# Kernel tuning notes

Hardware: AMD Instinct MI355X
Metric: run time of the kernel (lower is better)

Reference implementation:

```python
import jax, jax.numpy as jnp
import numpy as np

B, N, E = 16, 8192, 131072
CIN, H, HL, C = 128, 128, 128, 10
K1 = -(-N // 2)    # ceil(0.5 * 8192) = 4096 nodes kept after pool1
K2 = -(-K1 // 2)   # ceil(0.5 * 4096) = 2048 nodes kept after pool2


def setup_inputs() -> dict:
    key = jax.random.key(0)
    ks = jax.random.split(key, 12)

    def w(k, shape, fan):
        return (jax.random.normal(k, shape, jnp.float32) / np.sqrt(fan)).astype(jnp.float32)

    return {
        "x": jax.random.normal(ks[0], (B, N, CIN), jnp.float32),
        "edge_index": jax.random.randint(ks[1], (B, 2, E), 0, N),
        "W1": w(ks[2], (CIN, H), CIN), "b1": jnp.zeros((H,), jnp.float32),
        "p1_wrel": w(ks[3], (H, 1), H), "p1_wroot": w(ks[4], (H, 1), H), "p1_b": jnp.zeros((1,), jnp.float32),
        "W2": w(ks[5], (H, H), H), "b2": jnp.zeros((H,), jnp.float32),
        "p2_wrel": w(ks[6], (H, 1), H), "p2_wroot": w(ks[7], (H, 1), H), "p2_b": jnp.zeros((1,), jnp.float32),
        "W3": w(ks[8], (H, H), H), "b3": jnp.zeros((H,), jnp.float32),
        "lin1_w": w(ks[9], (H, HL), H), "lin1_b": jnp.zeros((HL,), jnp.float32),
        "lin2_w": w(ks[10], (HL, C), HL), "lin2_b": jnp.zeros((C,), jnp.float32),
    }


def _gcn(x, src, dst, mask, W, b):
    # GCNConv with self-loops + symmetric deg^-1/2 normalization on the
    # mask-induced subgraph (removed nodes contribute zero edge weight).
    ew = mask[src] * mask[dst]                                    # [E]
    deg = jax.ops.segment_sum(ew, dst, num_segments=N) + mask     # self-loop weight = mask
    deg_safe = jnp.where(deg > 0, deg, 1.0)
    dinv = jnp.where(deg > 0, jax.lax.rsqrt(deg_safe), 0.0)
    xw = x @ W                                                    # [N,H]
    norm = dinv[src] * ew * dinv[dst]                             # [E]
    agg = jax.ops.segment_sum(xw[src] * norm[:, None], dst, num_segments=N)
    out = agg + xw * (dinv * dinv * mask)[:, None] + b
    return out * mask[:, None]


def _sag_pool(x, src, dst, mask, wrel, wroot, bb, k):
    # SAGPooling: GraphConv(H,1) score (sum aggregation), top-k over live
    # nodes, tanh-gated features. Node filtering == updating the mask.
    ew = mask[src] * mask[dst]
    agg = jax.ops.segment_sum(x[src] * ew[:, None], dst, num_segments=N)
    score = (agg @ wrel + x @ wroot + bb)[:, 0] * mask            # [N]
    _, idx = jax.lax.top_k(jnp.where(mask > 0, score, -jnp.inf), k)
    new_mask = jnp.zeros((N,), x.dtype).at[idx].set(1.0)
    return x * jnp.tanh(score)[:, None] * new_mask[:, None], new_mask


def reference(x, edge_index, W1, b1, p1_wrel, p1_wroot, p1_b,
              W2, b2, p2_wrel, p2_wroot, p2_b, W3, b3,
              lin1_w, lin1_b, lin2_w, lin2_b):
    def per_graph(xg, ei):
        src, dst = ei[0], ei[1]
        mask = jnp.ones((N,), xg.dtype)
        h = jax.nn.relu(_gcn(xg, src, dst, mask, W1, b1))
        h, mask = _sag_pool(h, src, dst, mask, p1_wrel, p1_wroot, p1_b, K1)
        h = jax.nn.relu(_gcn(h, src, dst, mask, W2, b2))
        h, mask = _sag_pool(h, src, dst, mask, p2_wrel, p2_wroot, p2_b, K2)
        h = jax.nn.relu(_gcn(h, src, dst, mask, W3, b3))
        return h.sum(0) / K2  # global mean pool over the K2 surviving nodes

    g = jax.vmap(per_graph)(x, edge_index)                        # [B,H]
    hh = jax.nn.relu(g @ lin1_w + lin1_b)
    logits = hh @ lin2_w + lin2_b
    return jax.nn.log_softmax(logits, axis=-1)
```

## Files before the change

kernel.cpp:

```cpp
#include <hip/hip_runtime.h>
#include <hip/hip_bf16.h>
#include <math.h>

constexpr int B  = 16;
constexpr int N  = 8192;
constexpr int E  = 131072;
constexpr int H  = 128;
constexpr int K1 = 4096;
constexpr int K2 = 2048;

constexpr int CHUNKS = 16;
constexpr int NBK    = 16;
constexpr int FCAP   = 12288;

typedef __attribute__((ext_vector_type(8))) short short8;
typedef __attribute__((ext_vector_type(4))) float floatx4;

__device__ __forceinline__ unsigned short f2bf(float f) {
  unsigned u = __float_as_uint(f);
  return (unsigned short)((u + 0x7FFFu + ((u >> 16) & 1u)) >> 16);
}
__device__ __forceinline__ float bf2f(unsigned short s) {
  return __uint_as_float(((unsigned)s) << 16);
}
__device__ __forceinline__ int rdlane_i(int v, int l) {
  return __builtin_amdgcn_readlane(v, l);
}
__device__ __forceinline__ float rdlane_f(float v, int l) {
  return __uint_as_float((unsigned)__builtin_amdgcn_readlane((int)__float_as_uint(v), l));
}
__device__ __forceinline__ unsigned cvt_pk_bf16(float a, float b) {
  unsigned r;
  asm("v_cvt_pk_bf16_f32 %0, %1, %2" : "=v"(r) : "v"(a), "v"(b));
  return r;
}

__global__ __launch_bounds__(256) void hist_pass(const int* __restrict__ ei,
                                                 int* __restrict__ bchist) {
  int blk = blockIdx.x;
  int b = blk >> 4, c = blk & 15;
  __shared__ int h16[NBK];
  if (threadIdx.x < NBK) h16[threadIdx.x] = 0;
  __syncthreads();
  const int* dstp = ei + (size_t)b * 2 * E + E + c * 8192;
  for (int i = 0; i < 32; ++i) {
    int dst = dstp[i * 256 + threadIdx.x];
    atomicAdd(&h16[dst >> 9], 1);
  }
  __syncthreads();
  if (threadIdx.x < NBK) bchist[(blk << 4) + threadIdx.x] = h16[threadIdx.x];
}

__global__ __launch_bounds__(256) void bucket_scan(const int* __restrict__ bchist,
                                                   int* __restrict__ cursor,
                                                   int* __restrict__ bbase,
                                                   const float* __restrict__ W1,
                                                   const float* __restrict__ W2,
                                                   const float* __restrict__ W3,
                                                   unsigned short* __restrict__ Wt) {
  if (blockIdx.x >= 16) {
    int w = blockIdx.x - 16;
    const float* W = (w == 0) ? W1 : (w == 1) ? W2 : W3;
    unsigned short* o = Wt + w * 128 * 128;
    for (int i = threadIdx.x; i < 128 * 128; i += 256) {
      int k = i >> 7, n = i & 127;
      o[n * 128 + k] = f2bf(W[i]);
    }
    return;
  }
  int b = blockIdx.x;
  int tid = threadIdx.x;
  int c = tid >> 4, k = tid & 15;
  __shared__ int arr[CHUNKS][NBK];
  __shared__ int base[NBK + 1];
  arr[c][k] = bchist[((b * CHUNKS + c) << 4) + k];
  __syncthreads();
  if (tid == 0) {
    int run = 0;
    for (int kk = 0; kk < NBK; ++kk) {
      base[kk] = run;
      int t = 0;
      for (int cc = 0; cc < CHUNKS; ++cc) t += arr[cc][kk];
      run += t;
    }
    base[NBK] = run;
  }
  __syncthreads();
  int pre = 0;
  for (int cc = 0; cc < c; ++cc) pre += arr[cc][k];
  cursor[((b * CHUNKS + c) << 4) + k] = base[k] + pre;
  if (tid < NBK + 1) bbase[b * (NBK + 1) + tid] = base[tid];
}

__global__ __launch_bounds__(256) void bin_scatter(const int* __restrict__ ei,
                                                   const int* __restrict__ cursor,
                                                   unsigned* __restrict__ pbuf) {
  int blk = blockIdx.x;
  int b = blk >> 4, c = blk & 15;
  __shared__ int gcur[NBK], lcnt[NBK], lfill[NBK];
  __shared__ int lbase[NBK + 1];
  __shared__ unsigned sbuf[2048];
  int tid = threadIdx.x;
  if (tid < NBK) gcur[tid] = cursor[(blk << 4) + tid];
  const int* srcp = ei + (size_t)b * 2 * E + c * 8192;
  const int* dstp = srcp + E;
  unsigned* pb = pbuf + (size_t)b * E;

  for (int sc = 0; sc < 4; ++sc) {
    if (tid < NBK) { lcnt[tid] = 0; lfill[tid] = 0; }
    __syncthreads();
    int s8[8], d8[8];
#pragma unroll
    for (int q = 0; q < 8; ++q) {
      int i = sc * 2048 + q * 256 + tid;
      s8[q] = srcp[i]; d8[q] = dstp[i];
      atomicAdd(&lcnt[d8[q] >> 9], 1);
    }
    __syncthreads();
    if (tid == 0) {
      int run = 0;
      for (int k = 0; k < NBK; ++k) { lbase[k] = run; run += lcnt[k]; }
      lbase[NBK] = run;
    }
    __syncthreads();
#pragma unroll
    for (int q = 0; q < 8; ++q) {
      int k = d8[q] >> 9;
      int idx = atomicAdd(&lfill[k], 1);
      sbuf[lbase[k] + idx] = ((unsigned)k << 22) |
                             ((unsigned)(d8[q] & 511) << 13) | (unsigned)s8[q];
    }
    __syncthreads();
    for (int i = tid; i < 2048; i += 256) {
      unsigned pk = sbuf[i];
      int k = (int)(pk >> 22);
      pb[gcur[k] + (i - lbase[k])] = pk;
    }
    __syncthreads();
    if (tid < NBK) gcur[tid] += lcnt[tid];
    __syncthreads();
  }
}

__global__ __launch_bounds__(256) void final_scatter(const unsigned* __restrict__ pbuf,
                                                     const int* __restrict__ bbase,
                                                     int* __restrict__ csr,
                                                     int* __restrict__ offs,
                                                     float* __restrict__ dinv1) {
  int blk = blockIdx.x;
  int b = blk >> 4, k = blk & 15;
  __shared__ int ncnt[512], nbase[512], nfill[512];
  __shared__ int sred[256];
  __shared__ unsigned sbuf[FCAP];
  int tid = threadIdx.x;
  int gbase = bbase[b * (NBK + 1) + k];
  int gend  = bbase[b * (NBK + 1) + k + 1];
  int cnt = gend - gbase;
  const unsigned* pb = pbuf + (size_t)b * E + gbase;

  for (int i = tid; i < 512; i += 256) { ncnt[i] = 0; nfill[i] = 0; }
  __syncthreads();
  for (int i = tid; i < cnt; i += 256) atomicAdd(&ncnt[(pb[i] >> 13) & 511], 1);
  __syncthreads();
  int v0 = ncnt[2 * tid], v1 = ncnt[2 * tid + 1];
  int s = v0 + v1;
  sred[tid] = s;
  __syncthreads();
  for (int off = 1; off < 256; off <<= 1) {
    int x = (tid >= off) ? sred[tid - off] : 0;
    __syncthreads();
    sred[tid] += x;
    __syncthreads();
  }
  int ex = sred[tid] - s;
  nbase[2 * tid] = ex;
  nbase[2 * tid + 1] = ex + v0;
  __syncthreads();
  for (int i = tid; i < 512; i += 256) {
    int node = k * 512 + i;
    offs[b * (N + 1) + node] = gbase + nbase[i];
    dinv1[b * N + node] = rsqrtf((float)ncnt[i] + 1.0f);
  }
  if (k == 15 && tid == 0) offs[b * (N + 1) + N] = E;
  __syncthreads();
  for (int i = tid; i < cnt; i += 256) {
    unsigned pk = pb[i];
    int node = (pk >> 13) & 511;
    int idx = atomicAdd(&nfill[node], 1);
    sbuf[nbase[node] + idx] = pk & 8191u;
  }
  __syncthreads();
  int* co = csr + (size_t)b * E + gbase;
  for (int i = tid; i < cnt; i += 256) co[i] = (int)sbuf[i];
}

template <bool ABF16>
__global__ __launch_bounds__(256) void gemm_mfma(const void* __restrict__ Ap,
                                                 const unsigned short* __restrict__ Wt,
                                                 unsigned short* __restrict__ Cb,
                                                 const float* __restrict__ fscale,
                                                 const float* __restrict__ dscale) {
  __shared__ unsigned short Wsh[128 * 128];
  int tid  = threadIdx.x;
  int lane = tid & 63;
  int l15  = lane & 15, lg = lane >> 4;
  size_t rowbase = (size_t)blockIdx.x * 128 + (tid >> 6) * 32;

#pragma unroll
  for (int i = 0; i < 8; ++i) {
    int idx = tid + i * 256;
    int row = idx >> 4, s = idx & 15;
    short8 v = *(const short8*)(Wt + idx * 8);
    *(short8*)(Wsh + row * 128 + (s ^ (row & 15)) * 8) = v;
  }

  short8 afrag[2][4];
#pragma unroll
  for (int rg = 0; rg < 2; ++rg) {
    size_t row = rowbase + rg * 16 + l15;
#pragma unroll
    for (int c = 0; c < 4; ++c) {
      int k0 = c * 32 + lg * 8;
      if (ABF16) {
        afrag[rg][c] = *(const short8*)((const unsigned short*)Ap + row * 128 + k0);
      } else {
        const float* p = (const float*)Ap + row * 128 + k0;
        float4 v0 = *(const float4*)p;
        float4 v1 = *(const float4*)(p + 4);
        short8 a;
        a[0] = (short)f2bf(v0.x); a[1] = (short)f2bf(v0.y);
        a[2] = (short)f2bf(v0.z); a[3] = (short)f2bf(v0.w);
        a[4] = (short)f2bf(v1.x); a[5] = (short)f2bf(v1.y);
        a[6] = (short)f2bf(v1.z); a[7] = (short)f2bf(v1.w);
        afrag[rg][c] = a;
      }
    }
  }

  float fsr0[4] = {1.f, 1.f, 1.f, 1.f}, fsr1[4] = {1.f, 1.f, 1.f, 1.f};
  if (fscale != nullptr) {
    float4 t0 = *(const float4*)(fscale + rowbase + lg * 4);
    float4 t1 = *(const float4*)(fscale + rowbase + 16 + lg * 4);
    fsr0[0] = t0.x; fsr0[1] = t0.y; fsr0[2] = t0.z; fsr0[3] = t0.w;
    fsr1[0] = t1.x; fsr1[1] = t1.y; fsr1[2] = t1.z; fsr1[3] = t1.w;
  }
  if (dscale != nullptr) {
    float4 t0 = *(const float4*)(dscale + rowbase + lg * 4);
    float4 t1 = *(const float4*)(dscale + rowbase + 16 + lg * 4);
    fsr0[0] *= t0.x; fsr0[1] *= t0.y; fsr0[2] *= t0.z; fsr0[3] *= t0.w;
    fsr1[0] *= t1.x; fsr1[1] *= t1.y; fsr1[2] *= t1.z; fsr1[3] *= t1.w;
  }

  __syncthreads();

#pragma unroll
  for (int t = 0; t < 8; ++t) {
    int col = t * 16 + l15;
    short8 bfrag[4];
#pragma unroll
    for (int c = 0; c < 4; ++c)
      bfrag[c] = *(const short8*)(Wsh + col * 128 + ((c * 4 + lg) ^ (col & 15)) * 8);

    floatx4 acc0 = {0.f, 0.f, 0.f, 0.f};
    floatx4 acc1 = {0.f, 0.f, 0.f, 0.f};
#pragma unroll
    for (int c = 0; c < 4; ++c) {
      acc0 = __builtin_amdgcn_mfma_f32_16x16x32_bf16(afrag[0][c], bfrag[c], acc0, 0, 0, 0);
      acc1 = __builtin_amdgcn_mfma_f32_16x16x32_bf16(afrag[1][c], bfrag[c], acc1, 0, 0, 0);
    }
#pragma unroll
    for (int r = 0; r < 4; ++r) {
      size_t row0 = rowbase + lg * 4 + r;
      size_t row1 = rowbase + 16 + lg * 4 + r;
      Cb[row0 * 128 + col] = f2bf(acc0[r] * fsr0[r]);
      Cb[row1 * 128 + col] = f2bf(acc1[r] * fsr1[r]);
    }
  }
}

template <bool ALL_LIVE>
__global__ __launch_bounds__(256) void gcn_agg8(
    const unsigned* __restrict__ tmp, const float* __restrict__ dinv,
    const int* __restrict__ offs, const int* __restrict__ ecnt,
    const int* __restrict__ csr, const float* __restrict__ bias,
    unsigned* __restrict__ hout,
    const float* __restrict__ wrel, const float* __restrict__ wroot,
    float* __restrict__ rr, float* __restrict__ tt) {
  int blk = blockIdx.x;
  int xcd = blk & 7;
  int j   = blk >> 3;
  int b   = xcd * 2 + (j >> 11);
  int n   = (j & 2047) * 4 + (threadIdx.x >> 6);
  int wid = b * N + n;
  int lane = threadIdx.x & 63;

  float dv = rdlane_f(dinv[wid], 0);
  unsigned* hrow = hout + (size_t)wid * 64;

  if (!ALL_LIVE && dv <= 0.0f) {
    hrow[lane] = 0u;
    if (rr != nullptr && lane == 0) { rr[wid] = 0.0f; tt[wid] = 0.0f; }
    return;
  }

  const unsigned* tmpb = tmp + (((size_t)b << 13) << 6);
  const int* cs = csr + (size_t)b * E;

  float2 accA, accB;
  {
    unsigned u = tmpb[((unsigned)n << 6) + lane];
    accA.x = __uint_as_float(u << 16);
    accA.y = __uint_as_float(u & 0xFFFF0000u);
    accB.x = 0.0f; accB.y = 0.0f;
  }

  int nbase = b * (N + 1) + n;
  int o0 = __builtin_amdgcn_readfirstlane(offs[nbase]);
  int d;
  if (ALL_LIVE) d = __builtin_amdgcn_readfirstlane(offs[nbase + 1]) - o0;
  else          d = __builtin_amdgcn_readfirstlane(ecnt[wid]);

  for (int base = 0; base < d; base += 64) {
    int nv = d - base; if (nv > 64) nv = 64;
    int sl = (lane < nv) ? cs[o0 + base + lane] : 0;

    int nfull = nv >> 4;
    for (int t = 0; t < nfull; ++t) {
      int i0 = t << 4;
      unsigned uu[16];
#pragma unroll
      for (int q = 0; q < 16; ++q) {
        int sq = rdlane_i(sl, i0 + q);
        uu[q] = tmpb[((unsigned)sq << 6) + lane];
      }
#pragma unroll
      for (int q = 0; q < 16; ++q) {
        float lo = __uint_as_float(uu[q] << 16);
        float hi = __uint_as_float(uu[q] & 0xFFFF0000u);
        if (q & 1) { accB.x += lo; accB.y += hi; }
        else       { accA.x += lo; accA.y += hi; }
      }
    }
    int rem = nv & 15;
    if (rem) {
      int i0 = nfull << 4;
      unsigned uu[16];
#pragma unroll
      for (int q = 0; q < 16; ++q) {
        int idx = i0 + q;
        int sq = rdlane_i(sl, idx < nv ? idx : 0);
        unsigned v = tmpb[((unsigned)sq << 6) + lane];
        uu[q] = (idx < nv) ? v : 0u;
      }
#pragma unroll
      for (int q = 0; q < 16; ++q) {
        float lo = __uint_as_float(uu[q] << 16);
        float hi = __uint_as_float(uu[q] & 0xFFFF0000u);
        if (q & 1) { accB.x += lo; accB.y += hi; }
        else       { accA.x += lo; accA.y += hi; }
      }
    }
  }

  float2 acc = {accA.x + accB.x, accA.y + accB.y};
  const float2 bb = *(const float2*)(bias + lane * 2);
  float2 outv;
  outv.x = fmaxf(dv * acc.x + bb.x, 0.0f);
  outv.y = fmaxf(dv * acc.y + bb.y, 0.0f);
  hrow[lane] = cvt_pk_bf16(outv.x, outv.y);

  if (rr != nullptr) {
    const float2 wr = *(const float2*)(wrel + lane * 2);
    const float2 wo = *(const float2*)(wroot + lane * 2);
    float pr = outv.x * wr.x + outv.y * wr.y;
    float pt = outv.x * wo.x + outv.y * wo.y;
#pragma unroll
    for (int dd = 32; dd > 0; dd >>= 1) {
      pr += __shfl_down(pr, dd);
      pt += __shfl_down(pt, dd);
    }
    if (lane == 0) { rr[wid] = pr; tt[wid] = pt; }
  }
}

__global__ __launch_bounds__(256) void compact_pool(
    const float* __restrict__ mask, const int* __restrict__ offs,
    const int* __restrict__ ecnt_in, int* __restrict__ csr,
    int* __restrict__ ecnt_out, float* __restrict__ dinv_out) {
  int wid = blockIdx.x * 4 + (threadIdx.x >> 6);
  int lane = threadIdx.x & 63;
  int b = wid >> 13, n = wid & (N - 1);
  float m = rdlane_f(mask[wid], 0);
  if (m <= 0.0f) {
    if (lane == 0) { ecnt_out[wid] = 0; dinv_out[wid] = 0.0f; }
    return;
  }
  int nb = b * (N + 1) + n;
  int o0 = __builtin_amdgcn_readfirstlane(offs[nb]);
  int din = (ecnt_in != nullptr)
                ? __builtin_amdgcn_readfirstlane(ecnt_in[wid])
                : __builtin_amdgcn_readfirstlane(offs[nb + 1]) - o0;
  int* cs = csr + (size_t)b * E;
  const float* mb = mask + b * N;
  int wpos = o0;
  for (int base = 0; base < din; base += 64) {
    int nv = din - base; if (nv > 64) nv = 64;
    int s = (lane < nv) ? cs[o0 + base + lane] : 0;
    bool alive = (lane < nv) && (mb[s] > 0.0f);
    unsigned long long bal = __ballot(alive);
    int idx = __popcll(bal & ((1ull << lane) - 1ull));
    if (alive) cs[wpos + idx] = s;
    wpos += __popcll(bal);
  }
  if (lane == 0) {
    int total = wpos - o0;
    ecnt_out[wid] = total;
    dinv_out[wid] = rsqrtf((float)total + 1.0f);
  }
}

__global__ __launch_bounds__(256) void score_agg(const float* __restrict__ r,
                                                 const float* __restrict__ t,
                                                 const float* __restrict__ pb,
                                                 const float* __restrict__ livep,
                                                 const int* __restrict__ offs,
                                                 const int* __restrict__ ecnt,
                                                 const int* __restrict__ csr,
                                                 float* __restrict__ score) {
  int grp = threadIdx.x >> 4;
  int gl  = threadIdx.x & 15;
  int nid = blockIdx.x * 16 + grp;
  int b = nid >> 13, n = nid & (N - 1);
  bool live = (livep == nullptr) || (livep[nid] > 0.0f);
  float s = 0.0f;
  if (live) {
    int o0 = offs[b * (N + 1) + n];
    int d = (ecnt != nullptr) ? ecnt[nid] : offs[b * (N + 1) + n + 1] - o0;
    const int* cs = csr + (size_t)b * E;
    const float* rb = r + b * N;
    for (int base = 0; base < d; base += 16)
      if (base + gl < d) s += rb[cs[o0 + base + gl]];
  }
#pragma unroll
  for (int dd = 8; dd > 0; dd >>= 1) s += __shfl_xor(s, dd, 16);
  if (gl == 0) score[nid] = live ? (s + t[nid] + pb[0]) : 0.0f;
}

__device__ __forceinline__ unsigned fkey(float s, float m) {
  if (m <= 0.0f) return 0u;
  unsigned u = __float_as_uint(s);
  return (u & 0x80000000u) ? ~u : (u | 0x80000000u);
}

__global__ __launch_bounds__(1024) void topk_kernel(const float* __restrict__ score,
                                                    const float* __restrict__ mkin,
                                                    float* __restrict__ mkout,
                                                    float* __restrict__ fscale,
                                                    int k) {
  int b = blockIdx.x, tid = threadIdx.x;
  const float* sc = score + b * N;
  float* mk = mkout + b * N;
  float* fs = fscale + b * N;
  __shared__ unsigned keyb[N];
  __shared__ int hist[256];
  __shared__ unsigned sh_prefix;
  __shared__ int sh_kneed;
  __shared__ int wsum[16], wexc[16];

  for (int i = tid; i < N; i += 1024) {
    float m = (mkin == nullptr) ? 1.0f : mkin[b * N + i];
    keyb[i] = fkey(sc[i], m);
  }
  __syncthreads();

  unsigned prefix = 0, hm = 0;
  int kneed = k;
  for (int shift = 24; shift >= 0; shift -= 8) {
    if (tid < 256) hist[tid] = 0;
    __syncthreads();
    for (int i = tid; i < N; i += 1024) {
      unsigned key = keyb[i];
      if ((key & hm) == prefix) atomicAdd(&hist[(key >> shift) & 255], 1);
    }
    __syncthreads();
    if (tid < 64) {
      int b4[4]; int s = 0;
#pragma unroll
      for (int j = 0; j < 4; ++j) { b4[j] = hist[tid * 4 + j]; s += b4[j]; }
      int suf = s;
#pragma unroll
      for (int o = 1; o < 64; o <<= 1) {
        int v = __shfl_down(suf, o);
        if (tid + o < 64) suf += v;
      }
      int run = suf - s;
      for (int j = 3; j >= 0; --j) {
        if (run < kneed && run + b4[j] >= kneed) {
          sh_prefix = prefix | ((unsigned)(tid * 4 + j) << shift);
          sh_kneed = kneed - run;
        }
        run += b4[j];
      }
    }
    __syncthreads();
    prefix = sh_prefix;
    kneed = sh_kneed;
    hm |= (0xFFu << shift);
  }

  unsigned T = prefix;
  int base = tid * 8;
  unsigned keys[8];
  int eqf[8];
  int cnt = 0;
#pragma unroll
  for (int q = 0; q < 8; ++q) {
    keys[q] = keyb[base + q];
    eqf[q] = (keys[q] == T) ? 1 : 0;
    cnt += eqf[q];
  }
  int inc = cnt;
  int wl = tid & 63;
#pragma unroll
  for (int o = 1; o < 64; o <<= 1) {
    int v = __shfl_up(inc, o);
    if (wl >= o) inc += v;
  }
  if (wl == 63) wsum[tid >> 6] = inc;
  __syncthreads();
  if (tid < 16) {
    int v = wsum[tid];
    int in = v;
#pragma unroll
    for (int o = 1; o < 16; o <<= 1) {
      int u = __shfl_up(in, o);
      if (tid >= o) in += u;
    }
    wexc[tid] = in - v;
  }
  __syncthreads();
  int ex = wexc[tid >> 6] + (inc - cnt);
#pragma unroll
  for (int q = 0; q < 8; ++q) {
    bool sel = (keys[q] > T) || (eqf[q] && (ex < kneed));
    ex += eqf[q];
    mk[base + q] = sel ? 1.0f : 0.0f;
    fs[base + q] = sel ? tanhf(sc[base + q]) : 0.0f;
  }
}

__global__ __launch_bounds__(256) void readout(const unsigned short* __restrict__ h,
                                               float* __restrict__ part) {
  int b = blockIdx.x, c = blockIdx.y;
  int tid = threadIdx.x;
  int f = tid & 127, half = tid >> 7;
  float acc = 0.0f;
  for (int n = c * 256 + half; n < (c + 1) * 256; n += 2)
    acc += bf2f(h[((size_t)b * N + n) * 128 + f]);
  __shared__ float red[256];
  red[tid] = acc; __syncthreads();
  if (half == 0) part[((size_t)b * 32 + c) * 128 + f] = red[f] + red[f + 128];
}

__global__ __launch_bounds__(128) void head(const float* __restrict__ part,
                                            const float* __restrict__ l1w,
                                            const float* __restrict__ l1b,
                                            const float* __restrict__ l2w,
                                            const float* __restrict__ l2b,
                                            float* __restrict__ out) {
  int b = blockIdx.x, f = threadIdx.x;
  float g = 0.0f;
  for (int c = 0; c < 32; ++c) g += part[((size_t)b * 32 + c) * 128 + f];
  g *= (1.0f / (float)K2);
  __shared__ float gs[128], hh[128], lg[10];
  gs[f] = g; __syncthreads();
  float a = l1b[f];
  for (int kk = 0; kk < 128; ++kk) a += gs[kk] * l1w[kk * 128 + f];
  hh[f] = fmaxf(a, 0.0f); __syncthreads();
  if (f < 10) {
    float l = l2b[f];
    for (int j = 0; j < 128; ++j) l += hh[j] * l2w[j * 10 + f];
    lg[f] = l;
  }
  __syncthreads();
  if (f == 0) {
    float m = lg[0];
    for (int c = 1; c < 10; ++c) m = fmaxf(m, lg[c]);
    float s = 0.0f;
    for (int c = 0; c < 10; ++c) s += expf(lg[c] - m);
    float lse = m + logf(s);
    for (int c = 0; c < 10; ++c) out[b * 10 + c] = lg[c] - lse;
  }
}

extern "C" void kernel_launch(void* const* d_in, const int* in_sizes, int n_in,
                              void* d_out, int out_size, void* d_ws, size_t ws_size,
                              hipStream_t stream) {
  (void)in_sizes; (void)n_in; (void)out_size; (void)ws_size;
  const float* x       = (const float*)d_in[0];
  const int*   ei      = (const int*)d_in[1];
  const float* W1      = (const float*)d_in[2];
  const float* b1      = (const float*)d_in[3];
  const float* p1_wrel = (const float*)d_in[4];
  const float* p1_wroot= (const float*)d_in[5];
  const float* p1_b    = (const float*)d_in[6];
  const float* W2      = (const float*)d_in[7];
  const float* b2      = (const float*)d_in[8];
  const float* p2_wrel = (const float*)d_in[9];
  const float* p2_wroot= (const float*)d_in[10];
  const float* p2_b    = (const float*)d_in[11];
  const float* W3      = (const float*)d_in[12];
  const float* b3      = (const float*)d_in[13];
  const float* l1w     = (const float*)d_in[14];
  const float* l1b     = (const float*)d_in[15];
  const float* l2w     = (const float*)d_in[16];
  const float* l2b     = (const float*)d_in[17];
  float* out = (float*)d_out;

  char* p = (char*)d_ws;
  auto alloc = [&](size_t bytes) {
    char* r = p;
    p += ((bytes + 255) & ~(size_t)255);
    return r;
  };
  unsigned short* h   = (unsigned short*)alloc((size_t)B * N * H * 2);
  unsigned short* tmp = (unsigned short*)alloc((size_t)B * N * H * 2);
  int*      offs   = (int*)alloc((size_t)B * (N + 1) * 4);
  int*      csr    = (int*)alloc((size_t)B * E * 4);
  unsigned* pbuf   = (unsigned*)alloc((size_t)B * E * 4);
  int*      bchist = (int*)alloc((size_t)B * CHUNKS * NBK * 4);
  int*      cursor = (int*)alloc((size_t)B * CHUNKS * NBK * 4);
  int*      bbase  = (int*)alloc((size_t)B * (NBK + 1) * 4);
  int*      ecnt   = (int*)alloc((size_t)B * N * 4);
  float* dinv   = (float*)alloc((size_t)B * N * 4);
  float* mask   = (float*)alloc((size_t)B * N * 4);
  float* rr     = (float*)alloc((size_t)B * N * 4);
  float* tt     = (float*)alloc((size_t)B * N * 4);
  float* score  = (float*)alloc((size_t)B * N * 4);
  float* fscale = (float*)alloc((size_t)B * N * 4);
  float* part   = (float*)alloc((size_t)B * 32 * H * 4);
  unsigned short* Wts = (unsigned short*)alloc(3 * 128 * 128 * 2);

  hist_pass<<<B * CHUNKS, 256, 0, stream>>>(ei, bchist);
  bucket_scan<<<19, 256, 0, stream>>>(bchist, cursor, bbase, W1, W2, W3, Wts);
  bin_scatter<<<B * CHUNKS, 256, 0, stream>>>(ei, cursor, pbuf);
  final_scatter<<<B * NBK, 256, 0, stream>>>(pbuf, bbase, csr, offs, dinv);

  gemm_mfma<false><<<(B * N) / 128, 256, 0, stream>>>(x, Wts, tmp, nullptr, dinv);
  gcn_agg8<true><<<B * N / 4, 256, 0, stream>>>((const unsigned*)tmp, dinv, offs,
                                                nullptr, csr, b1, (unsigned*)h,
                                                p1_wrel, p1_wroot, rr, tt);
  score_agg<<<B * N / 16, 256, 0, stream>>>(rr, tt, p1_b, nullptr, offs, nullptr,
                                            csr, score);
  topk_kernel<<<B, 1024, 0, stream>>>(score, nullptr, mask, fscale, K1);
  compact_pool<<<B * N / 4, 256, 0, stream>>>(mask, offs, nullptr, csr, ecnt, dinv);

  gemm_mfma<true><<<(B * N) / 128, 256, 0, stream>>>(h, Wts + 128 * 128, tmp,
                                                     fscale, dinv);
  gcn_agg8<false><<<B * N / 4, 256, 0, stream>>>((const unsigned*)tmp, dinv, offs,
                                                 ecnt, csr, b2, (unsigned*)h,
                                                 p2_wrel, p2_wroot, rr, tt);
  score_agg<<<B * N / 16, 256, 0, stream>>>(rr, tt, p2_b, dinv, offs, ecnt, csr, score);
  topk_kernel<<<B, 1024, 0, stream>>>(score, mask, mask, fscale, K2);
  compact_pool<<<B * N / 4, 256, 0, stream>>>(mask, offs, ecnt, csr, ecnt, dinv);

  gemm_mfma<true><<<(B * N) / 128, 256, 0, stream>>>(h, Wts + 2 * 128 * 128, tmp,
                                                     fscale, dinv);
  gcn_agg8<false><<<B * N / 4, 256, 0, stream>>>((const unsigned*)tmp, dinv, offs,
                                                 ecnt, csr, b3, (unsigned*)h,
                                                 nullptr, nullptr, nullptr, nullptr);

  readout<<<dim3(B, 32), 256, 0, stream>>>(h, part);
  head<<<B, 128, 0, stream>>>(part, l1w, l1b, l2w, l2b, out);
}
```

Measured before the change: 392.4 us.

## Launch pooled stages only over surviving nodes via top-k index lists

```diff
diff --git a/kernel.cpp b/kernel.cpp
--- a/kernel.cpp
+++ b/kernel.cpp
@@ -194,12 +194,10 @@
   for (int i = tid; i < cnt; i += 256) co[i] = (int)sbuf[i];
 }
 
-template <bool ABF16>
-__global__ __launch_bounds__(256) void gemm_mfma(const void* __restrict__ Ap,
-                                                 const unsigned short* __restrict__ Wt,
-                                                 unsigned short* __restrict__ Cb,
-                                                 const float* __restrict__ fscale,
-                                                 const float* __restrict__ dscale) {
+__global__ __launch_bounds__(256) void gemm_l1(const float* __restrict__ Ap,
+                                               const unsigned short* __restrict__ Wt,
+                                               unsigned short* __restrict__ Cb,
+                                               const float* __restrict__ dscale) {
   __shared__ unsigned short Wsh[128 * 128];
   int tid  = threadIdx.x;
   int lane = tid & 63;
@@ -220,35 +218,24 @@
     size_t row = rowbase + rg * 16 + l15;
 #pragma unroll
     for (int c = 0; c < 4; ++c) {
-      int k0 = c * 32 + lg * 8;
-      if (ABF16) {
-        afrag[rg][c] = *(const short8*)((const unsigned short*)Ap + row * 128 + k0);
-      } else {
-        const float* p = (const float*)Ap + row * 128 + k0;
-        float4 v0 = *(const float4*)p;
-        float4 v1 = *(const float4*)(p + 4);
-        short8 a;
-        a[0] = (short)f2bf(v0.x); a[1] = (short)f2bf(v0.y);
-        a[2] = (short)f2bf(v0.z); a[3] = (short)f2bf(v0.w);
-        a[4] = (short)f2bf(v1.x); a[5] = (short)f2bf(v1.y);
-        a[6] = (short)f2bf(v1.z); a[7] = (short)f2bf(v1.w);
-        afrag[rg][c] = a;
-      }
-    }
-  }
-
-  float fsr0[4] = {1.f, 1.f, 1.f, 1.f}, fsr1[4] = {1.f, 1.f, 1.f, 1.f};
-  if (fscale != nullptr) {
-    float4 t0 = *(const float4*)(fscale + rowbase + lg * 4);
-    float4 t1 = *(const float4*)(fscale + rowbase + 16 + lg * 4);
+      const float* p = Ap + row * 128 + c * 32 + lg * 8;
+      float4 v0 = *(const float4*)p;
+      float4 v1 = *(const float4*)(p + 4);
+      short8 a;
+      a[0] = (short)f2bf(v0.x); a[1] = (short)f2bf(v0.y);
+      a[2] = (short)f2bf(v0.z); a[3] = (short)f2bf(v0.w);
+      a[4] = (short)f2bf(v1.x); a[5] = (short)f2bf(v1.y);
+      a[6] = (short)f2bf(v1.z); a[7] = (short)f2bf(v1.w);
+      afrag[rg][c] = a;
+    }
+  }
+
+  float fsr0[4], fsr1[4];
+  {
+    float4 t0 = *(const float4*)(dscale + rowbase + lg * 4);
+    float4 t1 = *(const float4*)(dscale + rowbase + 16 + lg * 4);
     fsr0[0] = t0.x; fsr0[1] = t0.y; fsr0[2] = t0.z; fsr0[3] = t0.w;
     fsr1[0] = t1.x; fsr1[1] = t1.y; fsr1[2] = t1.z; fsr1[3] = t1.w;
-  }
-  if (dscale != nullptr) {
-    float4 t0 = *(const float4*)(dscale + rowbase + lg * 4);
-    float4 t1 = *(const float4*)(dscale + rowbase + 16 + lg * 4);
-    fsr0[0] *= t0.x; fsr0[1] *= t0.y; fsr0[2] *= t0.z; fsr0[3] *= t0.w;
-    fsr1[0] *= t1.x; fsr1[1] *= t1.y; fsr1[2] *= t1.z; fsr1[3] *= t1.w;
   }
 
   __syncthreads();
@@ -278,12 +265,83 @@
   }
 }
 
-template <bool ALL_LIVE>
-__global__ __launch_bounds__(256) void gcn_agg8(
+template <int LGB>
+__global__ __launch_bounds__(256) void gemm_idx(const unsigned short* __restrict__ Ab,
+                                                const unsigned short* __restrict__ Wt,
+                                                unsigned short* __restrict__ Cb,
+                                                const float* __restrict__ fscale,
+                                                const float* __restrict__ dscale,
+                                                const int* __restrict__ idxl) {
+  __shared__ unsigned short Wsh[128 * 128];
+  __shared__ int ridx[128];
+  int tid  = threadIdx.x;
+  int lane = tid & 63;
+  int l15  = lane & 15, lg = lane >> 4;
+  int b    = blockIdx.x >> LGB;
+  int lblk = blockIdx.x & ((1 << LGB) - 1);
+  int woff = (tid >> 6) * 32;
+
+  if (tid < 128) ridx[tid] = idxl[b * N + lblk * 128 + tid];
+#pragma unroll
+  for (int i = 0; i < 8; ++i) {
+    int idx = tid + i * 256;
+    int row = idx >> 4, s = idx & 15;
+    short8 v = *(const short8*)(Wt + idx * 8);
+    *(short8*)(Wsh + row * 128 + (s ^ (row & 15)) * 8) = v;
+  }
+  __syncthreads();
+
+  const unsigned short* Ag = Ab + (size_t)b * N * 128;
+  unsigned short* Cg = Cb + (size_t)b * N * 128;
+  const float* fsb = fscale + b * N;
+  const float* dsb = dscale + b * N;
+
+  short8 afrag[2][4];
+#pragma unroll
+  for (int rg = 0; rg < 2; ++rg) {
+    int arow = ridx[woff + rg * 16 + l15];
+#pragma unroll
+    for (int c = 0; c < 4; ++c)
+      afrag[rg][c] = *(const short8*)(Ag + (size_t)arow * 128 + c * 32 + lg * 8);
+  }
+
+  int orow[2][4]; float fsr[2][4];
+#pragma unroll
+  for (int rg = 0; rg < 2; ++rg)
+#pragma unroll
+    for (int r = 0; r < 4; ++r) {
+      int o = ridx[woff + rg * 16 + lg * 4 + r];
+      orow[rg][r] = o;
+      fsr[rg][r] = fsb[o] * dsb[o];
+    }
+
+#pragma unroll
+  for (int t = 0; t < 8; ++t) {
+    int col = t * 16 + l15;
+    short8 bfrag[4];
+#pragma unroll
+    for (int c = 0; c < 4; ++c)
+      bfrag[c] = *(const short8*)(Wsh + col * 128 + ((c * 4 + lg) ^ (col & 15)) * 8);
+
+    floatx4 acc0 = {0.f, 0.f, 0.f, 0.f};
+    floatx4 acc1 = {0.f, 0.f, 0.f, 0.f};
+#pragma unroll
+    for (int c = 0; c < 4; ++c) {
+      acc0 = __builtin_amdgcn_mfma_f32_16x16x32_bf16(afrag[0][c], bfrag[c], acc0, 0, 0, 0);
+      acc1 = __builtin_amdgcn_mfma_f32_16x16x32_bf16(afrag[1][c], bfrag[c], acc1, 0, 0, 0);
+    }
+#pragma unroll
+    for (int r = 0; r < 4; ++r) {
+      Cg[(size_t)orow[0][r] * 128 + col] = f2bf(acc0[r] * fsr[0][r]);
+      Cg[(size_t)orow[1][r] * 128 + col] = f2bf(acc1[r] * fsr[1][r]);
+    }
+  }
+}
+
+__global__ __launch_bounds__(256) void gcn_agg_l1(
     const unsigned* __restrict__ tmp, const float* __restrict__ dinv,
-    const int* __restrict__ offs, const int* __restrict__ ecnt,
-    const int* __restrict__ csr, const float* __restrict__ bias,
-    unsigned* __restrict__ hout,
+    const int* __restrict__ offs, const int* __restrict__ csr,
+    const float* __restrict__ bias, unsigned* __restrict__ hout,
     const float* __restrict__ wrel, const float* __restrict__ wroot,
     float* __restrict__ rr, float* __restrict__ tt) {
   int blk = blockIdx.x;
@@ -297,12 +355,6 @@
   float dv = rdlane_f(dinv[wid], 0);
   unsigned* hrow = hout + (size_t)wid * 64;
 
-  if (!ALL_LIVE && dv <= 0.0f) {
-    hrow[lane] = 0u;
-    if (rr != nullptr && lane == 0) { rr[wid] = 0.0f; tt[wid] = 0.0f; }
-    return;
-  }
-
   const unsigned* tmpb = tmp + (((size_t)b << 13) << 6);
   const int* cs = csr + (size_t)b * E;
 
@@ -316,14 +368,11 @@
 
   int nbase = b * (N + 1) + n;
   int o0 = __builtin_amdgcn_readfirstlane(offs[nbase]);
-  int d;
-  if (ALL_LIVE) d = __builtin_amdgcn_readfirstlane(offs[nbase + 1]) - o0;
-  else          d = __builtin_amdgcn_readfirstlane(ecnt[wid]);
+  int d  = __builtin_amdgcn_readfirstlane(offs[nbase + 1]) - o0;
 
   for (int base = 0; base < d; base += 64) {
     int nv = d - base; if (nv > 64) nv = 64;
     int sl = (lane < nv) ? cs[o0 + base + lane] : 0;
-
     int nfull = nv >> 4;
     for (int t = 0; t < nfull; ++t) {
       int i0 = t << 4;
@@ -369,7 +418,108 @@
   outv.y = fmaxf(dv * acc.y + bb.y, 0.0f);
   hrow[lane] = cvt_pk_bf16(outv.x, outv.y);
 
-  if (rr != nullptr) {
+  const float2 wr = *(const float2*)(wrel + lane * 2);
+  const float2 wo = *(const float2*)(wroot + lane * 2);
+  float pr = outv.x * wr.x + outv.y * wr.y;
+  float pt = outv.x * wo.x + outv.y * wo.y;
+#pragma unroll
+  for (int dd = 32; dd > 0; dd >>= 1) {
+    pr += __shfl_down(pr, dd);
+    pt += __shfl_down(pt, dd);
+  }
+  if (lane == 0) { rr[wid] = pr; tt[wid] = pt; }
+}
+
+template <int LOGPG, bool FUSE_RO>
+__global__ __launch_bounds__(256) void gcn_agg_idx(
+    const unsigned* __restrict__ tmp, const float* __restrict__ dinv,
+    const int* __restrict__ offs, const int* __restrict__ ecnt,
+    const int* __restrict__ csr, const float* __restrict__ bias,
+    unsigned* __restrict__ hout, const float* __restrict__ wrel,
+    const float* __restrict__ wroot, float* __restrict__ rr,
+    float* __restrict__ tt, const int* __restrict__ idxl,
+    float* __restrict__ gacc) {
+  __shared__ float racc[128];
+  int blk = blockIdx.x;
+  int xcd = blk & 7;
+  int j   = blk >> 3;
+  int b   = xcd * 2 + (j >> LOGPG);
+  int i   = (j & ((1 << LOGPG) - 1)) * 4 + (threadIdx.x >> 6);
+  int lane = threadIdx.x & 63;
+
+  if (FUSE_RO) {
+    if (threadIdx.x < 128) racc[threadIdx.x] = 0.0f;
+    __syncthreads();
+  }
+
+  int n = __builtin_amdgcn_readfirstlane(idxl[b * N + i]);
+  int wid = b * N + n;
+  float dv = rdlane_f(dinv[wid], 0);
+
+  const unsigned* tmpb = tmp + (((size_t)b << 13) << 6);
+  const int* cs = csr + (size_t)b * E;
+
+  float2 accA, accB;
+  {
+    unsigned u = tmpb[((unsigned)n << 6) + lane];
+    accA.x = __uint_as_float(u << 16);
+    accA.y = __uint_as_float(u & 0xFFFF0000u);
+    accB.x = 0.0f; accB.y = 0.0f;
+  }
+
+  int o0 = __builtin_amdgcn_readfirstlane(offs[b * (N + 1) + n]);
+  int d  = __builtin_amdgcn_readfirstlane(ecnt[wid]);
+
+  for (int base = 0; base < d; base += 64) {
+    int nv = d - base; if (nv > 64) nv = 64;
+    int sl = (lane < nv) ? cs[o0 + base + lane] : 0;
+    int nfull = nv >> 4;
+    for (int t = 0; t < nfull; ++t) {
+      int i0 = t << 4;
+      unsigned uu[16];
+#pragma unroll
+      for (int q = 0; q < 16; ++q) {
+        int sq = rdlane_i(sl, i0 + q);
+        uu[q] = tmpb[((unsigned)sq << 6) + lane];
+      }
+#pragma unroll
+      for (int q = 0; q < 16; ++q) {
+        float lo = __uint_as_float(uu[q] << 16);
+        float hi = __uint_as_float(uu[q] & 0xFFFF0000u);
+        if (q & 1) { accB.x += lo; accB.y += hi; }
+        else       { accA.x += lo; accA.y += hi; }
+      }
+    }
+    int rem = nv & 15;
+    if (rem) {
+      int i0 = nfull << 4;
+      unsigned uu[16];
+#pragma unroll
+      for (int q = 0; q < 16; ++q) {
+        int idx = i0 + q;
+        int sq = rdlane_i(sl, idx < nv ? idx : 0);
+        unsigned v = tmpb[((unsigned)sq << 6) + lane];
+        uu[q] = (idx < nv) ? v : 0u;
+      }
+#pragma unroll
+      for (int q = 0; q < 16; ++q) {
+        float lo = __uint_as_float(uu[q] << 16);
+        float hi = __uint_as_float(uu[q] & 0xFFFF0000u);
+        if (q & 1) { accB.x += lo; accB.y += hi; }
+        else       { accA.x += lo; accA.y += hi; }
+      }
+    }
+  }
+
+  float2 acc = {accA.x + accB.x, accA.y + accB.y};
+  const float2 bb = *(const float2*)(bias + lane * 2);
+  float2 outv;
+  outv.x = fmaxf(dv * acc.x + bb.x, 0.0f);
+  outv.y = fmaxf(dv * acc.y + bb.y, 0.0f);
+
+  if (!FUSE_RO) {
+    unsigned* hrow = hout + (size_t)wid * 64;
+    hrow[lane] = cvt_pk_bf16(outv.x, outv.y);
     const float2 wr = *(const float2*)(wrel + lane * 2);
     const float2 wo = *(const float2*)(wroot + lane * 2);
     float pr = outv.x * wr.x + outv.y * wr.y;
@@ -380,21 +530,26 @@
       pt += __shfl_down(pt, dd);
     }
     if (lane == 0) { rr[wid] = pr; tt[wid] = pt; }
-  }
-}
-
-__global__ __launch_bounds__(256) void compact_pool(
-    const float* __restrict__ mask, const int* __restrict__ offs,
-    const int* __restrict__ ecnt_in, int* __restrict__ csr,
-    int* __restrict__ ecnt_out, float* __restrict__ dinv_out) {
-  int wid = blockIdx.x * 4 + (threadIdx.x >> 6);
+  } else {
+    atomicAdd(&racc[lane * 2],     outv.x);
+    atomicAdd(&racc[lane * 2 + 1], outv.y);
+    __syncthreads();
+    if (threadIdx.x < 128) atomicAdd(&gacc[b * 128 + threadIdx.x], racc[threadIdx.x]);
+  }
+}
+
+template <int LOGK>
+__global__ __launch_bounds__(256) void compact_idx(
+    const int* __restrict__ idxl, const float* __restrict__ mask,
+    const int* __restrict__ offs, const int* __restrict__ ecnt_in,
+    int* __restrict__ csr, int* __restrict__ ecnt_out,
+    float* __restrict__ dinv_out) {
+  int ws = blockIdx.x * 4 + (threadIdx.x >> 6);
+  int b = ws >> LOGK;
+  int i = ws & ((1 << LOGK) - 1);
   int lane = threadIdx.x & 63;
-  int b = wid >> 13, n = wid & (N - 1);
-  float m = rdlane_f(mask[wid], 0);
-  if (m <= 0.0f) {
-    if (lane == 0) { ecnt_out[wid] = 0; dinv_out[wid] = 0.0f; }
-    return;
-  }
+  int n = __builtin_amdgcn_readfirstlane(idxl[b * N + i]);
+  int wid = b * N + n;
   int nb = b * (N + 1) + n;
   int o0 = __builtin_amdgcn_readfirstlane(offs[nb]);
   int din = (ecnt_in != nullptr)
@@ -419,31 +574,52 @@
   }
 }
 
-__global__ __launch_bounds__(256) void score_agg(const float* __restrict__ r,
-                                                 const float* __restrict__ t,
-                                                 const float* __restrict__ pb,
-                                                 const float* __restrict__ livep,
-                                                 const int* __restrict__ offs,
-                                                 const int* __restrict__ ecnt,
-                                                 const int* __restrict__ csr,
-                                                 float* __restrict__ score) {
+__global__ __launch_bounds__(256) void score_l1(const float* __restrict__ r,
+                                                const float* __restrict__ t,
+                                                const float* __restrict__ pb,
+                                                const int* __restrict__ offs,
+                                                const int* __restrict__ csr,
+                                                float* __restrict__ score) {
   int grp = threadIdx.x >> 4;
   int gl  = threadIdx.x & 15;
   int nid = blockIdx.x * 16 + grp;
   int b = nid >> 13, n = nid & (N - 1);
-  bool live = (livep == nullptr) || (livep[nid] > 0.0f);
+  int o0 = offs[b * (N + 1) + n], o1 = offs[b * (N + 1) + n + 1];
+  const int* cs = csr + (size_t)b * E;
+  const float* rb = r + b * N;
   float s = 0.0f;
-  if (live) {
-    int o0 = offs[b * (N + 1) + n];
-    int d = (ecnt != nullptr) ? ecnt[nid] : offs[b * (N + 1) + n + 1] - o0;
-    const int* cs = csr + (size_t)b * E;
-    const float* rb = r + b * N;
-    for (int base = 0; base < d; base += 16)
-      if (base + gl < d) s += rb[cs[o0 + base + gl]];
-  }
+  for (int base = o0; base < o1; base += 16)
+    if (base + gl < o1) s += rb[cs[base + gl]];
 #pragma unroll
   for (int dd = 8; dd > 0; dd >>= 1) s += __shfl_xor(s, dd, 16);
-  if (gl == 0) score[nid] = live ? (s + t[nid] + pb[0]) : 0.0f;
+  if (gl == 0) score[nid] = s + t[nid] + pb[0];
+}
+
+__global__ __launch_bounds__(256) void score_idx(const float* __restrict__ r,
+                                                 const float* __restrict__ t,
+                                                 const float* __restrict__ pb,
+                                                 const int* __restrict__ offs,
+                                                 const int* __restrict__ ecnt,
+                                                 const int* __restrict__ csr,
+                                                 float* __restrict__ score,
+                                                 const int* __restrict__ idxl) {
+  int grp = threadIdx.x >> 4;
+  int gl  = threadIdx.x & 15;
+  int ws  = blockIdx.x * 16 + grp;
+  int b = ws >> 12;
+  int i = ws & (K1 - 1);
+  int n = idxl[b * N + i];
+  int nid = b * N + n;
+  int o0 = offs[b * (N + 1) + n];
+  int d  = ecnt[nid];
+  const int* cs = csr + (size_t)b * E;
+  const float* rb = r + b * N;
+  float s = 0.0f;
+  for (int base = 0; base < d; base += 16)
+    if (base + gl < d) s += rb[cs[o0 + base + gl]];
+#pragma unroll
+  for (int dd = 8; dd > 0; dd >>= 1) s += __shfl_xor(s, dd, 16);
+  if (gl == 0) score[nid] = s + t[nid] + pb[0];
 }
 
 __device__ __forceinline__ unsigned fkey(float s, float m) {
@@ -456,6 +632,7 @@
                                                     const float* __restrict__ mkin,
                                                     float* __restrict__ mkout,
                                                     float* __restrict__ fscale,
+                                                    int* __restrict__ idxo,
                                                     int k) {
   int b = blockIdx.x, tid = threadIdx.x;
   const float* sc = score + b * N;
@@ -540,38 +717,50 @@
   }
   __syncthreads();
   int ex = wexc[tid >> 6] + (inc - cnt);
+  int scnt = 0; bool selq[8];
 #pragma unroll
   for (int q = 0; q < 8; ++q) {
     bool sel = (keys[q] > T) || (eqf[q] && (ex < kneed));
     ex += eqf[q];
     mk[base + q] = sel ? 1.0f : 0.0f;
     fs[base + q] = sel ? tanhf(sc[base + q]) : 0.0f;
-  }
-}
-
-__global__ __launch_bounds__(256) void readout(const unsigned short* __restrict__ h,
-                                               float* __restrict__ part) {
-  int b = blockIdx.x, c = blockIdx.y;
-  int tid = threadIdx.x;
-  int f = tid & 127, half = tid >> 7;
-  float acc = 0.0f;
-  for (int n = c * 256 + half; n < (c + 1) * 256; n += 2)
-    acc += bf2f(h[((size_t)b * N + n) * 128 + f]);
-  __shared__ float red[256];
-  red[tid] = acc; __syncthreads();
-  if (half == 0) part[((size_t)b * 32 + c) * 128 + f] = red[f] + red[f + 128];
-}
-
-__global__ __launch_bounds__(128) void head(const float* __restrict__ part,
+    selq[q] = sel; scnt += sel;
+  }
+  int inc2 = scnt;
+#pragma unroll
+  for (int o = 1; o < 64; o <<= 1) {
+    int v = __shfl_up(inc2, o);
+    if (wl >= o) inc2 += v;
+  }
+  __syncthreads();
+  if (wl == 63) wsum[tid >> 6] = inc2;
+  __syncthreads();
+  if (tid < 16) {
+    int v = wsum[tid];
+    int in = v;
+#pragma unroll
+    for (int o = 1; o < 16; o <<= 1) {
+      int u = __shfl_up(in, o);
+      if (tid >= o) in += u;
+    }
+    wexc[tid] = in - v;
+  }
+  __syncthreads();
+  int spos = wexc[tid >> 6] + (inc2 - scnt);
+  int* io = idxo + b * N;
+#pragma unroll
+  for (int q = 0; q < 8; ++q)
+    if (selq[q]) io[spos++] = base + q;
+}
+
+__global__ __launch_bounds__(128) void head(const float* __restrict__ gacc,
                                             const float* __restrict__ l1w,
                                             const float* __restrict__ l1b,
                                             const float* __restrict__ l2w,
                                             const float* __restrict__ l2b,
                                             float* __restrict__ out) {
   int b = blockIdx.x, f = threadIdx.x;
-  float g = 0.0f;
-  for (int c = 0; c < 32; ++c) g += part[((size_t)b * 32 + c) * 128 + f];
-  g *= (1.0f / (float)K2);
+  float g = gacc[b * 128 + f] * (1.0f / (float)K2);
   __shared__ float gs[128], hh[128], lg[10];
   gs[f] = g; __syncthreads();
   float a = l1b[f];
@@ -632,44 +821,47 @@
   int*      cursor = (int*)alloc((size_t)B * CHUNKS * NBK * 4);
   int*      bbase  = (int*)alloc((size_t)B * (NBK + 1) * 4);
   int*      ecnt   = (int*)alloc((size_t)B * N * 4);
+  int*      idx1   = (int*)alloc((size_t)B * N * 4);
+  int*      idx2   = (int*)alloc((size_t)B * N * 4);
   float* dinv   = (float*)alloc((size_t)B * N * 4);
   float* mask   = (float*)alloc((size_t)B * N * 4);
   float* rr     = (float*)alloc((size_t)B * N * 4);
   float* tt     = (float*)alloc((size_t)B * N * 4);
   float* score  = (float*)alloc((size_t)B * N * 4);
   float* fscale = (float*)alloc((size_t)B * N * 4);
-  float* part   = (float*)alloc((size_t)B * 32 * H * 4);
+  float* gacc   = (float*)alloc((size_t)B * 128 * 4);
   unsigned short* Wts = (unsigned short*)alloc(3 * 128 * 128 * 2);
 
   hist_pass<<<B * CHUNKS, 256, 0, stream>>>(ei, bchist);
   bucket_scan<<<19, 256, 0, stream>>>(bchist, cursor, bbase, W1, W2, W3, Wts);
   bin_scatter<<<B * CHUNKS, 256, 0, stream>>>(ei, cursor, pbuf);
   final_scatter<<<B * NBK, 256, 0, stream>>>(pbuf, bbase, csr, offs, dinv);
-
-  gemm_mfma<false><<<(B * N) / 128, 256, 0, stream>>>(x, Wts, tmp, nullptr, dinv);
-  gcn_agg8<true><<<B * N / 4, 256, 0, stream>>>((const unsigned*)tmp, dinv, offs,
-                                                nullptr, csr, b1, (unsigned*)h,
-                                                p1_wrel, p1_wroot, rr, tt);
-  score_agg<<<B * N / 16, 256, 0, stream>>>(rr, tt, p1_b, nullptr, offs, nullptr,
-                                            csr, score);
-  topk_kernel<<<B, 1024, 0, stream>>>(score, nullptr, mask, fscale, K1);
-  compact_pool<<<B * N / 4, 256, 0, stream>>>(mask, offs, nullptr, csr, ecnt, dinv);
-
-  gemm_mfma<true><<<(B * N) / 128, 256, 0, stream>>>(h, Wts + 128 * 128, tmp,
-                                                     fscale, dinv);
-  gcn_agg8<false><<<B * N / 4, 256, 0, stream>>>((const unsigned*)tmp, dinv, offs,
-                                                 ecnt, csr, b2, (unsigned*)h,
-                                                 p2_wrel, p2_wroot, rr, tt);
-  score_agg<<<B * N / 16, 256, 0, stream>>>(rr, tt, p2_b, dinv, offs, ecnt, csr, score);
-  topk_kernel<<<B, 1024, 0, stream>>>(score, mask, mask, fscale, K2);
-  compact_pool<<<B * N / 4, 256, 0, stream>>>(mask, offs, ecnt, csr, ecnt, dinv);
-
-  gemm_mfma<true><<<(B * N) / 128, 256, 0, stream>>>(h, Wts + 2 * 128 * 128, tmp,
-                                                     fscale, dinv);
-  gcn_agg8<false><<<B * N / 4, 256, 0, stream>>>((const unsigned*)tmp, dinv, offs,
-                                                 ecnt, csr, b3, (unsigned*)h,
-                                                 nullptr, nullptr, nullptr, nullptr);
-
-  readout<<<dim3(B, 32), 256, 0, stream>>>(h, part);
-  head<<<B, 128, 0, stream>>>(part, l1w, l1b, l2w, l2b, out);
-}
+  hipMemsetAsync(gacc, 0, (size_t)B * 128 * 4, stream);
+
+  gemm_l1<<<(B * N) / 128, 256, 0, stream>>>(x, Wts, tmp, dinv);
+  gcn_agg_l1<<<B * N / 4, 256, 0, stream>>>((const unsigned*)tmp, dinv, offs, csr, b1,
+                                            (unsigned*)h, p1_wrel, p1_wroot, rr, tt);
+  score_l1<<<B * N / 16, 256, 0, stream>>>(rr, tt, p1_b, offs, csr, score);
+  topk_kernel<<<B, 1024, 0, stream>>>(score, nullptr, mask, fscale, idx1, K1);
+  compact_idx<12><<<B * K1 / 4, 256, 0, stream>>>(idx1, mask, offs, nullptr, csr,
+                                                  ecnt, dinv);
+
+  gemm_idx<5><<<B * (K1 / 128), 256, 0, stream>>>(h, Wts + 128 * 128, tmp,
+                                                  fscale, dinv, idx1);
+  gcn_agg_idx<10, false><<<B * K1 / 4, 256, 0, stream>>>(
+      (const unsigned*)tmp, dinv, offs, ecnt, csr, b2, (unsigned*)h,
+      p2_wrel, p2_wroot, rr, tt, idx1, nullptr);
+  score_idx<<<B * K1 / 16, 256, 0, stream>>>(rr, tt, p2_b, offs, ecnt, csr,
+                                             score, idx1);
+  topk_kernel<<<B, 1024, 0, stream>>>(score, mask, mask, fscale, idx2, K2);
+  compact_idx<11><<<B * K2 / 4, 256, 0, stream>>>(idx2, mask, offs, ecnt, csr,
+                                                  ecnt, dinv);
+
+  gemm_idx<4><<<B * (K2 / 128), 256, 0, stream>>>(h, Wts + 2 * 128 * 128, tmp,
+                                                  fscale, dinv, idx2);
+  gcn_agg_idx<9, true><<<B * K2 / 4, 256, 0, stream>>>(
+      (const unsigned*)tmp, dinv, offs, ecnt, csr, b3, nullptr,
+      nullptr, nullptr, nullptr, nullptr, idx2, gacc);
+
+  head<<<B, 128, 0, stream>>>(gacc, l1w, l1b, l2w, l2b, out);
+}
```

New measurement: 327.5 us. 16.5% less time.
